# Performance work log

Hardware: AMD Instinct MI355X
Metric: run time of the kernel (lower is better)

## Reference

```python
import jax, jax.numpy as jnp
import numpy as np

ALPHA = 2.0  # spikingjelly default ATan surrogate alpha
EPS = 1e-5   # BatchNorm eps

@jax.custom_vjp
def heaviside_atan(x):
    return (x >= 0.0).astype(x.dtype)

def _ha_fwd(x):
    return heaviside_atan(x), x

def _ha_bwd(x, g):
    return (g * ALPHA / (2.0 * (1.0 + (jnp.pi / 2.0 * ALPHA * x) ** 2)),)

heaviside_atan.defvjp(_ha_fwd, _ha_bwd)

def lif(x_seq, tau=2.0, v_th=1.0):
    # MultiStepLIFNode, v_reset=0 (hard reset), detach_reset=True
    def step(v, x):
        v = v + (x - v) / tau
        s = heaviside_atan(v - v_th)
        v = v * (1.0 - jax.lax.stop_gradient(s))
        return v, s
    _, spikes = jax.lax.scan(step, jnp.zeros_like(x_seq[0]), x_seq)
    return spikes

def conv_bn(y, Wt, g, b):
    # 1x1 conv (no bias) + BatchNorm2d in training mode over flattened (T*B, H, W)
    y = jnp.einsum('tbchw,oc->tbohw', y, Wt)
    m = y.mean(axis=(0, 1, 3, 4), keepdims=True)
    v = y.var(axis=(0, 1, 3, 4), keepdims=True)
    C = Wt.shape[0]
    return (y - m) / jnp.sqrt(v + EPS) * g.reshape(1, 1, C, 1, 1) + b.reshape(1, 1, C, 1, 1)

def setup_inputs() -> dict:
    key = jax.random.key(0)
    ks = jax.random.split(key, 5)
    T, B, C, H, W = 4, 64, 384, 14, 14
    x = jax.random.normal(ks[0], (T, B, C, H, W), dtype=jnp.float32)
    Wq = jax.random.normal(ks[1], (C, C), dtype=jnp.float32) * 0.02
    Wk = jax.random.normal(ks[2], (C, C), dtype=jnp.float32) * 0.02
    Wv = jax.random.normal(ks[3], (C, C), dtype=jnp.float32) * 0.02
    Wp = jax.random.normal(ks[4], (C, C), dtype=jnp.float32) * 0.02
    ones = jnp.ones((C,), jnp.float32)
    zeros = jnp.zeros((C,), jnp.float32)
    return {"x": x, "Wq": Wq, "Wk": Wk, "Wv": Wv, "Wp": Wp,
            "gq": ones, "bq": zeros, "gk": ones, "bk": zeros,
            "gv": ones, "bv": zeros, "gp": ones, "bp": zeros}

def reference(x, Wq, Wk, Wv, Wp, gq, bq, gk, bk, gv, bv, gp, bp):
    T, B, C, H, W = x.shape
    nh = 8
    dh = C // nh
    N = H * W

    xs = lif(x)  # pre_lif

    def heads(y):  # [T,B,C,H,W] -> [T,B,h,N,dh]
        y = y.reshape(T, B, C, N).transpose(0, 1, 3, 2)
        return y.reshape(T, B, N, nh, dh).transpose(0, 1, 3, 2, 4)

    q = heads(lif(conv_bn(xs, Wq, gq, bq)))
    k = heads(lif(conv_bn(xs, Wk, gk, bk)))
    v = heads(lif(conv_bn(xs, Wv, gv, bv)))

    attn = jnp.einsum('tbhnd,tbhmd->tbhnm', q, k)      # no softmax
    o = jnp.einsum('tbhnm,tbhmd->tbhnd', attn, v) * 0.125
    o = o.transpose(0, 1, 2, 4, 3).reshape(T, B, C, N).reshape(T, B, C, H, W)
    o = lif(o, v_th=0.5)                                # attn_lif
    return conv_bn(o, Wp, gp, bp)                       # proj (no lif)
```

## Files before the change

### kernel.cpp

```cpp
#include <hip/hip_runtime.h>
#include <hip/hip_bf16.h>
#include <stdint.h>

#define T_  4
#define B_  64
#define C_  384
#define N_  196
#define NH  8
#define DH  48
#define TB_ (T_*B_)
#define R_  (T_*B_*N_)
#define NW  12
#define P_  12544
#define SBLK1 3136
#define SA_  64

typedef float f32x2 __attribute__((ext_vector_type(2)));

__global__ void transpose_w4(const float* __restrict__ s0, const float* __restrict__ s1,
                             const float* __restrict__ s2, const float* __restrict__ s3,
                             float* __restrict__ dst){
    int m = blockIdx.y;
    const float* src = (m==0)?s0:(m==1)?s1:(m==2)?s2:s3;
    int idx = blockIdx.x*256 + threadIdx.x;
    if (idx >= C_*C_) return;
    int o = idx % C_, c = idx / C_;
    dst[(size_t)m*C_*C_ + idx] = src[o*C_ + c];
}

__global__ __launch_bounds__(256) void pre_lif(const float* __restrict__ x,
                                               uint32_t* __restrict__ maskXS){
    int b = blockIdx.x / NW;
    int w = blockIdx.x % NW;
    int n = threadIdx.x;
    if (n >= N_) return;
    float v[32];
#pragma unroll
    for (int j=0;j<32;j++) v[j] = 0.f;
#pragma unroll
    for (int t=0;t<T_;t++){
        uint32_t word = 0;
#pragma unroll
        for (int j=0;j<32;j++){
            int c = w*32 + j;
            float xv = x[((size_t)(t*B_+b)*C_ + c)*N_ + n];
            v[j] = v[j] + (xv - v[j])*0.5f;
            if (v[j] >= 1.0f){ word |= (1u<<j); v[j] = 0.f; }
        }
        maskXS[((size_t)(t*B_+b)*N_ + n)*NW + w] = word;
    }
}

__global__ __launch_bounds__(256) void conv_statsO(const uint32_t* __restrict__ mask,
                                                   const float* __restrict__ WT,
                                                   float* __restrict__ p1,
                                                   float* __restrict__ p2){
    __shared__ float red1[4][C_];
    __shared__ float red2[4][C_];
    int tid = threadIdx.x, wave = tid>>6, lane = tid&63;
    int ob = 6*lane;
    f32x2 s10={0.f,0.f}, s11={0.f,0.f}, s12={0.f,0.f};
    f32x2 s20={0.f,0.f}, s21={0.f,0.f}, s22={0.f,0.f};
    for (int p=0;p<4;p++){
        int pix = (blockIdx.x*4 + wave)*4 + p;
        const uint4* m4 = (const uint4*)(mask + (size_t)pix*NW);
        uint4 ma = m4[0], mb = m4[1], mc = m4[2];
        uint32_t mwv[12] = {ma.x,ma.y,ma.z,ma.w, mb.x,mb.y,mb.z,mb.w, mc.x,mc.y,mc.z,mc.w};
        f32x2 y0={0.f,0.f}, y1={0.f,0.f}, y2={0.f,0.f};
        f32x2 z0={0.f,0.f}, z1={0.f,0.f}, z2={0.f,0.f};
#pragma unroll
        for (int w=0; w<NW; w++){
            uint32_t bits = mwv[w];
            while (bits){
                int c0 = (w<<5) + __builtin_ctz(bits); bits &= bits-1;
                const f32x2* col0 = (const f32x2*)(WT + (size_t)c0*C_ + ob);
                if (bits){
                    int c1 = (w<<5) + __builtin_ctz(bits); bits &= bits-1;
                    const f32x2* col1 = (const f32x2*)(WT + (size_t)c1*C_ + ob);
                    f32x2 a0=col0[0],a1=col0[1],a2=col0[2];
                    f32x2 b0=col1[0],b1=col1[1],b2=col1[2];
                    y0+=a0; y1+=a1; y2+=a2;
                    z0+=b0; z1+=b1; z2+=b2;
                } else {
                    y0+=col0[0]; y1+=col0[1]; y2+=col0[2];
                }
            }
        }
        y0+=z0; y1+=z1; y2+=z2;
        s10+=y0; s11+=y1; s12+=y2;
        s20+=y0*y0; s21+=y1*y1; s22+=y2*y2;
    }
    *(f32x2*)&red1[wave][ob  ] = s10;
    *(f32x2*)&red1[wave][ob+2] = s11;
    *(f32x2*)&red1[wave][ob+4] = s12;
    *(f32x2*)&red2[wave][ob  ] = s20;
    *(f32x2*)&red2[wave][ob+2] = s21;
    *(f32x2*)&red2[wave][ob+4] = s22;
    __syncthreads();
    for (int i=tid; i<C_; i+=256){
        p1[(size_t)blockIdx.x*C_ + i] = (red1[0][i]+red1[1][i])+(red1[2][i]+red1[3][i]);
        p2[(size_t)blockIdx.x*C_ + i] = (red2[0][i]+red2[1][i])+(red2[2][i]+red2[3][i]);
    }
}

__global__ __launch_bounds__(384) void statsA(const float* __restrict__ p1,
                                              const float* __restrict__ p2,
                                              float* __restrict__ q1,
                                              float* __restrict__ q2){
    int o = threadIdx.x;
    int blk = blockIdx.x;
    const int ROWS = SBLK1 / SA_;
    size_t base = (size_t)blk*ROWS*C_ + o;
    float s1=0.f, s2=0.f;
#pragma unroll 4
    for (int r=0;r<ROWS;r++){
        s1 += p1[base + (size_t)r*C_];
        s2 += p2[base + (size_t)r*C_];
    }
    q1[blk*C_ + o] = s1;
    q2[blk*C_ + o] = s2;
}

__global__ __launch_bounds__(384) void statsB(const float* __restrict__ q1,
                                              const float* __restrict__ q2,
                                              const float* __restrict__ g,
                                              const float* __restrict__ bta,
                                              float* __restrict__ scale,
                                              float* __restrict__ shift){
    int o = threadIdx.x;
    float s1=0.f, s2=0.f;
#pragma unroll
    for (int b=0;b<SA_;b++){ s1 += q1[b*C_+o]; s2 += q2[b*C_+o]; }
    float m   = s1 / (float)R_;
    float var = s2 / (float)R_ - m*m;
    float sc  = g[o] / sqrtf(var + 1e-5f);
    scale[o] = sc;
    shift[o] = bta[o] - m*sc;
}

__global__ __launch_bounds__(256) void conv_lif(const uint32_t* __restrict__ mask,
                                                const float* __restrict__ WT,
                                                const float* __restrict__ scale,
                                                const float* __restrict__ shift,
                                                uint32_t* __restrict__ mo){
    int tid = threadIdx.x, wave = tid>>6, lane = tid&63;
    int pix0 = blockIdx.x*4 + wave;
    float sc[6], sh[6], v[6];
#pragma unroll
    for (int i=0;i<6;i++){
        sc[i] = scale[(i<<6)+lane];
        sh[i] = shift[(i<<6)+lane];
        v[i]  = 0.f;
    }
    for (int t=0;t<T_;t++){
        size_t pix = (size_t)t*P_ + pix0;
        const uint4* m4 = (const uint4*)(mask + pix*NW);
        uint4 ma = m4[0], mb = m4[1], mc = m4[2];
        uint32_t mwv[12] = {ma.x,ma.y,ma.z,ma.w, mb.x,mb.y,mb.z,mb.w, mc.x,mc.y,mc.z,mc.w};
        float y[6] = {0.f,0.f,0.f,0.f,0.f,0.f};
        float z[6] = {0.f,0.f,0.f,0.f,0.f,0.f};
#pragma unroll
        for (int w=0; w<NW; w++){
            uint32_t bits = mwv[w];
            while (bits){
                int c0 = (w<<5) + __builtin_ctz(bits); bits &= bits-1;
                const float* col0 = WT + (size_t)c0*C_ + lane;
                if (bits){
                    int c1 = (w<<5) + __builtin_ctz(bits); bits &= bits-1;
                    const float* col1 = WT + (size_t)c1*C_ + lane;
#pragma unroll
                    for (int i=0;i<6;i++){ y[i]+=col0[i<<6]; z[i]+=col1[i<<6]; }
                } else {
#pragma unroll
                    for (int i=0;i<6;i++) y[i]+=col0[i<<6];
                }
            }
        }
        uint32_t words[12];
#pragma unroll
        for (int i=0;i<6;i++){
            float val = (y[i]+z[i])*sc[i] + sh[i];
            v[i] = v[i] + (val - v[i])*0.5f;
            int s = (v[i] >= 1.0f);
            unsigned long long bal = __ballot(s);
            if (s) v[i] = 0.f;
            words[2*i]   = (uint32_t)bal;
            words[2*i+1] = (uint32_t)(bal>>32);
        }
        if (lane == 0){
            uint4* o4 = (uint4*)(mo + pix*NW);
            o4[0] = make_uint4(words[0],words[1],words[2],words[3]);
            o4[1] = make_uint4(words[4],words[5],words[6],words[7]);
            o4[2] = make_uint4(words[8],words[9],words[10],words[11]);
        }
    }
}

__global__ __launch_bounds__(256) void attention_lif(const uint32_t* __restrict__ mq,
                                                     const uint32_t* __restrict__ mk,
                                                     const uint32_t* __restrict__ mv,
                                                     uint16_t* __restrict__ mo){
    __shared__ unsigned long long kT[DH][4];
    __shared__ unsigned long long vT[DH][4];
    __shared__ uint32_t Cp[DH*25];

    int h = blockIdx.x & 7;
    int b = blockIdx.x >> 3;
    int tid = threadIdx.x, wv = tid>>6, lane = tid&63;
    int sw  = (h*DH) >> 5;
    int shf = (h*DH) & 31;

    float vm[DH];
#pragma unroll
    for (int d=0;d<DH;d++) vm[d] = 0.f;

    for (int t=0;t<T_;t++){
        int tb = t*B_ + b;
        unsigned long long q = 0, kk = 0, vvv = 0;
        if (tid < N_){
            const uint32_t* pq = mq + ((size_t)tb*N_ + tid)*NW + sw;
            const uint32_t* pk = mk + ((size_t)tb*N_ + tid)*NW + sw;
            const uint32_t* pv = mv + ((size_t)tb*N_ + tid)*NW + sw;
            unsigned long long lo, hi;
            lo = pq[0]; hi = pq[1];
            q   = (shf ? ((lo>>16) | (hi<<16)) : (lo | (hi<<32))) & 0xFFFFFFFFFFFFULL;
            lo = pk[0]; hi = pk[1];
            kk  = (shf ? ((lo>>16) | (hi<<16)) : (lo | (hi<<32))) & 0xFFFFFFFFFFFFULL;
            lo = pv[0]; hi = pv[1];
            vvv = (shf ? ((lo>>16) | (hi<<16)) : (lo | (hi<<32))) & 0xFFFFFFFFFFFFULL;
        }
#pragma unroll 1
        for (int d=0; d<DH; d++){
            unsigned long long bk_ = __ballot((int)((kk >>d)&1ull));
            unsigned long long bv_ = __ballot((int)((vvv>>d)&1ull));
            if (lane == 0){ kT[d][wv] = bk_; vT[d][wv] = bv_; }
        }
        __syncthreads();

        if (tid < 240){
            int j  = tid / 5;
            int dg = tid % 5;
            int d0 = dg*10;
            int d1 = (dg==4) ? 48 : d0+10;
            unsigned long long ka=kT[j][0], kb=kT[j][1], kc=kT[j][2], kd=kT[j][3];
            for (int d=d0; d<d1; d+=2){
                uint32_t c0 = (uint32_t)(__popcll(ka&vT[d][0]) + __popcll(kb&vT[d][1])
                            + __popcll(kc&vT[d][2]) + __popcll(kd&vT[d][3]));
                uint32_t c1 = (uint32_t)(__popcll(ka&vT[d+1][0]) + __popcll(kb&vT[d+1][1])
                            + __popcll(kc&vT[d+1][2]) + __popcll(kd&vT[d+1][3]));
                Cp[j*25 + (d>>1)] = c0 | (c1<<16);
            }
        }
        __syncthreads();

        if (tid < N_){
            uint32_t acc[24];
#pragma unroll
            for (int p=0;p<24;p++) acc[p] = 0u;
            unsigned long long qb = q;
            while (qb){
                int j = __builtin_ctzll(qb); qb &= qb-1;
                const uint32_t* row = &Cp[j*25];
#pragma unroll
                for (int p=0;p<24;p++) acc[p] += row[p];
            }
            unsigned long long sp = 0;
#pragma unroll
            for (int d=0; d<DH; d++){
                uint32_t a = (d&1) ? (acc[d>>1]>>16) : (acc[d>>1]&0xFFFFu);
                float o = 0.125f*(float)a;
                vm[d] = vm[d] + (o - vm[d])*0.5f;
                if (vm[d] >= 0.5f){ sp |= (1ull<<d); vm[d] = 0.f; }
            }
            size_t rec = ((size_t)tb*N_ + tid)*24 + 3*h;
            mo[rec]   = (uint16_t)(sp);
            mo[rec+1] = (uint16_t)(sp >> 16);
            mo[rec+2] = (uint16_t)(sp >> 32);
        }
        __syncthreads();
    }
}

__global__ __launch_bounds__(256) void proj_out(const uint32_t* __restrict__ mask,
                                                const float* __restrict__ WT,
                                                const float* __restrict__ scale,
                                                const float* __restrict__ shift,
                                                float* __restrict__ out){
    __shared__ float tile[192][98];
    int bid = blockIdx.x;
    int tb = bid>>2, nh = (bid>>1)&1, ch = bid&1;
    int n0 = nh*98, c0 = ch*192;
    int tid = threadIdx.x, wave = tid>>6, lane = tid&63;
    float sc[3], sh[3];
#pragma unroll
    for (int i=0;i<3;i++){
        sc[i] = scale[c0+(i<<6)+lane];
        sh[i] = shift[c0+(i<<6)+lane];
    }
    for (int p=wave; p<98; p+=4){
        size_t pix = (size_t)tb*N_ + n0 + p;
        const uint4* m4 = (const uint4*)(mask + pix*NW);
        uint4 ma = m4[0], mb = m4[1], mc = m4[2];
        uint32_t mwv[12] = {ma.x,ma.y,ma.z,ma.w, mb.x,mb.y,mb.z,mb.w, mc.x,mc.y,mc.z,mc.w};
        float y[3] = {0.f,0.f,0.f};
        float z[3] = {0.f,0.f,0.f};
#pragma unroll
        for (int w=0; w<NW; w++){
            uint32_t bits = mwv[w];
            while (bits){
                int cc0 = (w<<5) + __builtin_ctz(bits); bits &= bits-1;
                const float* col0 = WT + (size_t)cc0*C_ + c0 + lane;
                if (bits){
                    int cc1 = (w<<5) + __builtin_ctz(bits); bits &= bits-1;
                    const float* col1 = WT + (size_t)cc1*C_ + c0 + lane;
#pragma unroll
                    for (int i=0;i<3;i++){ y[i]+=col0[i<<6]; z[i]+=col1[i<<6]; }
                } else {
#pragma unroll
                    for (int i=0;i<3;i++) y[i]+=col0[i<<6];
                }
            }
        }
#pragma unroll
        for (int i=0;i<3;i++)
            tile[(i<<6)+lane][p] = (y[i]+z[i])*sc[i] + sh[i];
    }
    __syncthreads();
    for (int r=wave; r<192; r+=4){
        if (lane < 49){
            f32x2 tv = *(const f32x2*)&tile[r][2*lane];
            *(f32x2*)(out + ((size_t)tb*C_ + c0 + r)*N_ + n0 + 2*lane) = tv;
        }
    }
}

extern "C" void kernel_launch(void* const* d_in, const int* in_sizes, int n_in,
                              void* d_out, int out_size, void* d_ws, size_t ws_size,
                              hipStream_t stream) {
    const float* x  = (const float*)d_in[0];
    const float* Wq = (const float*)d_in[1];
    const float* Wk = (const float*)d_in[2];
    const float* Wv = (const float*)d_in[3];
    const float* Wp = (const float*)d_in[4];
    const float* gq = (const float*)d_in[5];
    const float* bq = (const float*)d_in[6];
    const float* gk = (const float*)d_in[7];
    const float* bk = (const float*)d_in[8];
    const float* gv = (const float*)d_in[9];
    const float* bv = (const float*)d_in[10];
    const float* gp = (const float*)d_in[11];
    const float* bp = (const float*)d_in[12];

    char* w = (char*)d_ws;
    size_t off = 0;
    uint32_t* maskXS = (uint32_t*)(w + off); off += (size_t)R_*NW*4;
    uint32_t* maskQ  = (uint32_t*)(w + off); off += (size_t)R_*NW*4;
    uint32_t* maskK  = (uint32_t*)(w + off); off += (size_t)R_*NW*4;
    uint32_t* maskV  = (uint32_t*)(w + off); off += (size_t)R_*NW*4;
    float* WTall = (float*)(w + off); off += (size_t)4*C_*C_*4;
    float* p1 = (float*)(w + off); off += (size_t)SBLK1*C_*4;
    float* p2 = (float*)(w + off); off += (size_t)SBLK1*C_*4;
    float* q1 = (float*)(w + off); off += (size_t)SA_*C_*4;
    float* q2 = (float*)(w + off); off += (size_t)SA_*C_*4;
    float* scaleB = (float*)(w + off); off += C_*4;
    float* shiftB = (float*)(w + off); off += C_*4;
    uint32_t* maskOL = maskXS;

    transpose_w4<<<dim3((C_*C_+255)/256, 4),256,0,stream>>>(Wq, Wk, Wv, Wp, WTall);

    pre_lif<<<B_*NW,256,0,stream>>>(x, maskXS);

    const float* Gs[3] = {gq, gk, gv};
    const float* Bs[3] = {bq, bk, bv};
    uint32_t* Ms[3] = {maskQ, maskK, maskV};
    for (int i=0;i<3;i++){
        const float* WT = WTall + (size_t)i*C_*C_;
        conv_statsO<<<SBLK1,256,0,stream>>>(maskXS, WT, p1, p2);
        statsA<<<SA_,384,0,stream>>>(p1, p2, q1, q2);
        statsB<<<1,384,0,stream>>>(q1, q2, Gs[i], Bs[i], scaleB, shiftB);
        conv_lif<<<P_/4,256,0,stream>>>(maskXS, WT, scaleB, shiftB, Ms[i]);
    }

    attention_lif<<<B_*NH,256,0,stream>>>(maskQ, maskK, maskV, (uint16_t*)maskOL);

    const float* WTp = WTall + (size_t)3*C_*C_;
    conv_statsO<<<SBLK1,256,0,stream>>>(maskOL, WTp, p1, p2);
    statsA<<<SA_,384,0,stream>>>(p1, p2, q1, q2);
    statsB<<<1,384,0,stream>>>(q1, q2, gp, bp, scaleB, shiftB);

    proj_out<<<TB_*4,256,0,stream>>>(maskOL, WTp, scaleB, shiftB, (float*)d_out);
}
```

Measured before the change: 445.8 us.

## Compute BatchNorm stats from binary spike Gram matrix instead of conv passes

Replaces the per-branch conv+stats passes with a bit-transposed spike mask and a popcount Gram matrix S^T S, shared by the Q/K/V branches. Mean and variance of each conv output channel then come from W·G·W^T and the spike counts, so the input is read once rather than three times. conv_lif is batched across the three branches in one launch, and both conv kernels now build a shared-memory list of active channel indices with 4-way accumulation. This adds new kernels, LDS atomics and a larger workspace. Computing variance as E[y^2]-m^2 in fp32 from Gram sums changes the rounding.

Result: faster. 422.6 us (-5.2%).

```diff
diff --git a/kernel.cpp b/kernel.cpp
--- a/kernel.cpp
+++ b/kernel.cpp
@@ -12,8 +12,8 @@
 #define R_  (T_*B_*N_)
 #define NW  12
 #define P_  12544
-#define SBLK1 3136
-#define SA_  64
+#define NCH 66
+#define KG_ 17
 
 typedef float f32x2 __attribute__((ext_vector_type(2)));
 
@@ -51,105 +51,149 @@
     }
 }
 
-__global__ __launch_bounds__(256) void conv_statsO(const uint32_t* __restrict__ mask,
-                                                   const float* __restrict__ WT,
-                                                   float* __restrict__ p1,
-                                                   float* __restrict__ p2){
-    __shared__ float red1[4][C_];
-    __shared__ float red2[4][C_];
+__global__ __launch_bounds__(256) void bit_transpose(const uint32_t* __restrict__ mask,
+                                                     unsigned long long* __restrict__ maskT){
+    int gw = blockIdx.x*4 + (threadIdx.x>>6);
+    int lane = threadIdx.x & 63;
+    int kc = gw/12, kw = gw%12;
+    uint32_t mwv[12];
+#pragma unroll
+    for (int w=0;w<12;w++) mwv[w]=0u;
+    if (gw < 784){
+        int pix = gw*64 + lane;
+        const uint4* m4 = (const uint4*)(mask + (size_t)pix*NW);
+        uint4 a=m4[0], b=m4[1], c=m4[2];
+        mwv[0]=a.x; mwv[1]=a.y; mwv[2]=a.z; mwv[3]=a.w;
+        mwv[4]=b.x; mwv[5]=b.y; mwv[6]=b.z; mwv[7]=b.w;
+        mwv[8]=c.x; mwv[9]=c.y; mwv[10]=c.z; mwv[11]=c.w;
+    }
+#pragma unroll
+    for (int w=0; w<12; w++){
+        uint32_t word = mwv[w];
+#pragma unroll
+        for (int j=0; j<32; j++){
+            unsigned long long bal = __ballot((int)((word>>j)&1u));
+            if (lane == 0)
+                maskT[((size_t)kc*C_ + (w*32+j))*12 + kw] = bal;
+        }
+    }
+}
+
+__global__ __launch_bounds__(256) void gram(const unsigned long long* __restrict__ maskT,
+                                            unsigned int* __restrict__ Gpart){
+    __shared__ unsigned int tile[64][49];
     int tid = threadIdx.x, wave = tid>>6, lane = tid&63;
-    int ob = 6*lane;
-    f32x2 s10={0.f,0.f}, s11={0.f,0.f}, s12={0.f,0.f};
-    f32x2 s20={0.f,0.f}, s21={0.f,0.f}, s22={0.f,0.f};
-    for (int p=0;p<4;p++){
-        int pix = (blockIdx.x*4 + wave)*4 + p;
-        const uint4* m4 = (const uint4*)(mask + (size_t)pix*NW);
-        uint4 ma = m4[0], mb = m4[1], mc = m4[2];
-        uint32_t mwv[12] = {ma.x,ma.y,ma.z,ma.w, mb.x,mb.y,mb.z,mb.w, mc.x,mc.y,mc.z,mc.w};
-        f32x2 y0={0.f,0.f}, y1={0.f,0.f}, y2={0.f,0.f};
-        f32x2 z0={0.f,0.f}, z1={0.f,0.f}, z2={0.f,0.f};
-#pragma unroll
-        for (int w=0; w<NW; w++){
-            uint32_t bits = mwv[w];
-            while (bits){
-                int c0 = (w<<5) + __builtin_ctz(bits); bits &= bits-1;
-                const f32x2* col0 = (const f32x2*)(WT + (size_t)c0*C_ + ob);
-                if (bits){
-                    int c1 = (w<<5) + __builtin_ctz(bits); bits &= bits-1;
-                    const f32x2* col1 = (const f32x2*)(WT + (size_t)c1*C_ + ob);
-                    f32x2 a0=col0[0],a1=col0[1],a2=col0[2];
-                    f32x2 b0=col1[0],b1=col1[1],b2=col1[2];
-                    y0+=a0; y1+=a1; y2+=a2;
-                    z0+=b0; z1+=b1; z2+=b2;
-                } else {
-                    y0+=col0[0]; y1+=col0[1]; y2+=col0[2];
-                }
-            }
-        }
-        y0+=z0; y1+=z1; y2+=z2;
-        s10+=y0; s11+=y1; s12+=y2;
-        s20+=y0*y0; s21+=y1*y1; s22+=y2*y2;
-    }
-    *(f32x2*)&red1[wave][ob  ] = s10;
-    *(f32x2*)&red1[wave][ob+2] = s11;
-    *(f32x2*)&red1[wave][ob+4] = s12;
-    *(f32x2*)&red2[wave][ob  ] = s20;
-    *(f32x2*)&red2[wave][ob+2] = s21;
-    *(f32x2*)&red2[wave][ob+4] = s22;
+    int kg = blockIdx.x, rg = blockIdx.y, cg = blockIdx.z;
+    for (int i=tid; i<64*49; i+=256) ((unsigned int*)tile)[i] = 0u;
     __syncthreads();
-    for (int i=tid; i<C_; i+=256){
-        p1[(size_t)blockIdx.x*C_ + i] = (red1[0][i]+red1[1][i])+(red1[2][i]+red1[3][i]);
-        p2[(size_t)blockIdx.x*C_ + i] = (red2[0][i]+red2[1][i])+(red2[2][i]+red2[3][i]);
-    }
-}
-
-__global__ __launch_bounds__(384) void statsA(const float* __restrict__ p1,
-                                              const float* __restrict__ p2,
-                                              float* __restrict__ q1,
-                                              float* __restrict__ q2){
-    int o = threadIdx.x;
-    int blk = blockIdx.x;
-    const int ROWS = SBLK1 / SA_;
-    size_t base = (size_t)blk*ROWS*C_ + o;
-    float s1=0.f, s2=0.f;
+    int kc = kg*4 + wave;
+    if (kc < NCH){
+        const uint4* rp = (const uint4*)(maskT + ((size_t)kc*C_ + rg*64 + lane)*12);
+        uint32_t row[24];
+#pragma unroll
+        for (int q=0;q<6;q++){
+            uint4 a = rp[q];
+            row[4*q]=a.x; row[4*q+1]=a.y; row[4*q+2]=a.z; row[4*q+3]=a.w;
+        }
+        for (int cc=0; cc<48; cc++){
+            const uint4* cp = (const uint4*)(maskT + ((size_t)kc*C_ + cg*48 + cc)*12);
+            uint32_t col[24];
+#pragma unroll
+            for (int q=0;q<6;q++){
+                uint4 a = cp[q];
+                col[4*q]=a.x; col[4*q+1]=a.y; col[4*q+2]=a.z; col[4*q+3]=a.w;
+            }
+            unsigned int s = 0;
+#pragma unroll
+            for (int q=0;q<24;q++) s += (unsigned int)__popc(row[q]&col[q]);
+            atomicAdd(&tile[lane][cc], s);
+        }
+    }
+    __syncthreads();
+    unsigned int* out = Gpart + (size_t)kg*C_*C_;
+    for (int i=tid; i<64*48; i+=256){
+        int r = i/48, cc = i%48;
+        out[(size_t)(rg*64+r)*C_ + cg*48 + cc] = tile[r][cc];
+    }
+}
+
+__global__ __launch_bounds__(256) void gram_reduce(const unsigned int* __restrict__ Gpart,
+                                                   float* __restrict__ Gf){
+    int e = blockIdx.x*256 + threadIdx.x;
+    unsigned int s = 0;
+#pragma unroll
+    for (int k=0;k<KG_;k++) s += Gpart[(size_t)k*C_*C_ + e];
+    Gf[e] = (float)s;
+}
+
+__global__ __launch_bounds__(384) void bn_from_gram(const float* __restrict__ Gf,
+        const float* __restrict__ WTall,
+        const float* __restrict__ g0, const float* __restrict__ b0,
+        const float* __restrict__ g1, const float* __restrict__ b1,
+        const float* __restrict__ g2, const float* __restrict__ b2,
+        float* __restrict__ scaleOut, float* __restrict__ shiftOut, int wtBase){
+    __shared__ float w4[384][4];
+    __shared__ float sred[8][6];
+    int t = threadIdx.x, wave = t>>6, lane = t&63;
+    int br = blockIdx.y;
+    const float* WT = WTall + (size_t)(wtBase+br)*C_*C_;
+    int o0 = blockIdx.x*4;
+    float4 wv = *(const float4*)(WT + (size_t)t*C_ + o0);
+    w4[t][0]=wv.x; w4[t][1]=wv.y; w4[t][2]=wv.z; w4[t][3]=wv.w;
+    __syncthreads();
+    float h0=0.f,h1=0.f,h2=0.f,h3=0.f;
 #pragma unroll 4
-    for (int r=0;r<ROWS;r++){
-        s1 += p1[base + (size_t)r*C_];
-        s2 += p2[base + (size_t)r*C_];
-    }
-    q1[blk*C_ + o] = s1;
-    q2[blk*C_ + o] = s2;
-}
-
-__global__ __launch_bounds__(384) void statsB(const float* __restrict__ q1,
-                                              const float* __restrict__ q2,
-                                              const float* __restrict__ g,
-                                              const float* __restrict__ bta,
-                                              float* __restrict__ scale,
-                                              float* __restrict__ shift){
-    int o = threadIdx.x;
-    float s1=0.f, s2=0.f;
-#pragma unroll
-    for (int b=0;b<SA_;b++){ s1 += q1[b*C_+o]; s2 += q2[b*C_+o]; }
-    float m   = s1 / (float)R_;
-    float var = s2 / (float)R_ - m*m;
-    float sc  = g[o] / sqrtf(var + 1e-5f);
-    scale[o] = sc;
-    shift[o] = bta[o] - m*sc;
+    for (int c=0;c<C_;c++){
+        float gv = Gf[(size_t)c*C_ + t];
+        float4 wc = *(const float4*)&w4[c][0];
+        h0 += gv*wc.x; h1 += gv*wc.y; h2 += gv*wc.z; h3 += gv*wc.w;
+    }
+    float cnt = Gf[(size_t)t*C_ + t];
+    float p0=wv.x*h0, p1=wv.y*h1, p2=wv.z*h2, p3=wv.w*h3;
+    float q0=cnt*wv.x, q1=cnt*wv.y, q2=cnt*wv.z, q3=cnt*wv.w;
+#pragma unroll
+    for (int off=32; off>0; off>>=1){
+        p0+=__shfl_down(p0,off); p1+=__shfl_down(p1,off);
+        p2+=__shfl_down(p2,off); p3+=__shfl_down(p3,off);
+        q0+=__shfl_down(q0,off); q1+=__shfl_down(q1,off);
+        q2+=__shfl_down(q2,off); q3+=__shfl_down(q3,off);
+    }
+    if (lane == 0){
+        sred[0][wave]=p0; sred[1][wave]=p1; sred[2][wave]=p2; sred[3][wave]=p3;
+        sred[4][wave]=q0; sred[5][wave]=q1; sred[6][wave]=q2; sred[7][wave]=q3;
+    }
+    __syncthreads();
+    if (t < 4){
+        const float* g  = (br==0)?g0:(br==1)?g1:g2;
+        const float* bb = (br==0)?b0:(br==1)?b1:b2;
+        float ss = ((sred[t][0]+sred[t][1])+(sred[t][2]+sred[t][3]))+(sred[t][4]+sred[t][5]);
+        float sm = ((sred[4+t][0]+sred[4+t][1])+(sred[4+t][2]+sred[4+t][3]))+(sred[4+t][4]+sred[4+t][5]);
+        float m   = sm / (float)R_;
+        float var = ss / (float)R_ - m*m;
+        float sc  = g[o0+t] / sqrtf(var + 1e-5f);
+        scaleOut[br*C_ + o0+t] = sc;
+        shiftOut[br*C_ + o0+t] = bb[o0+t] - m*sc;
+    }
 }
 
 __global__ __launch_bounds__(256) void conv_lif(const uint32_t* __restrict__ mask,
-                                                const float* __restrict__ WT,
-                                                const float* __restrict__ scale,
-                                                const float* __restrict__ shift,
-                                                uint32_t* __restrict__ mo){
+                                                const float* __restrict__ WTall,
+                                                const float* __restrict__ scaleAll,
+                                                const float* __restrict__ shiftAll,
+                                                uint32_t* __restrict__ moQ,
+                                                uint32_t* __restrict__ moK,
+                                                uint32_t* __restrict__ moV){
+    __shared__ uint16_t lst[4][400];
+    int br = blockIdx.y;
+    const float* WT = WTall + (size_t)br*C_*C_;
+    uint32_t* mo = (br==0)?moQ:(br==1)?moK:moV;
     int tid = threadIdx.x, wave = tid>>6, lane = tid&63;
     int pix0 = blockIdx.x*4 + wave;
     float sc[6], sh[6], v[6];
 #pragma unroll
     for (int i=0;i<6;i++){
-        sc[i] = scale[(i<<6)+lane];
-        sh[i] = shift[(i<<6)+lane];
+        sc[i] = scaleAll[br*C_ + (i<<6) + lane];
+        sh[i] = shiftAll[br*C_ + (i<<6) + lane];
         v[i]  = 0.f;
     }
     for (int t=0;t<T_;t++){
@@ -157,35 +201,51 @@
         const uint4* m4 = (const uint4*)(mask + pix*NW);
         uint4 ma = m4[0], mb = m4[1], mc = m4[2];
         uint32_t mwv[12] = {ma.x,ma.y,ma.z,ma.w, mb.x,mb.y,mb.z,mb.w, mc.x,mc.y,mc.z,mc.w};
-        float y[6] = {0.f,0.f,0.f,0.f,0.f,0.f};
-        float z[6] = {0.f,0.f,0.f,0.f,0.f,0.f};
-#pragma unroll
-        for (int w=0; w<NW; w++){
-            uint32_t bits = mwv[w];
-            while (bits){
-                int c0 = (w<<5) + __builtin_ctz(bits); bits &= bits-1;
-                const float* col0 = WT + (size_t)c0*C_ + lane;
-                if (bits){
-                    int c1 = (w<<5) + __builtin_ctz(bits); bits &= bits-1;
-                    const float* col1 = WT + (size_t)c1*C_ + lane;
-#pragma unroll
-                    for (int i=0;i<6;i++){ y[i]+=col0[i<<6]; z[i]+=col1[i<<6]; }
-                } else {
-#pragma unroll
-                    for (int i=0;i<6;i++) y[i]+=col0[i<<6];
+        int cnt = 0;
+#pragma unroll
+        for (int w=0;w<12;w++) cnt += __popc(mwv[w]);
+        if (lane == 0){
+            int k = 0;
+#pragma unroll
+            for (int w=0;w<12;w++){
+                uint32_t bits = mwv[w];
+                while (bits){
+                    lst[wave][k++] = (uint16_t)((w<<5) + __builtin_ctz(bits));
+                    bits &= bits - 1;
                 }
             }
         }
+        float ya[6]={0,0,0,0,0,0}, yb[6]={0,0,0,0,0,0};
+        float yc[6]={0,0,0,0,0,0}, yd[6]={0,0,0,0,0,0};
+        int i = 0;
+        for (; i+3 < cnt; i += 4){
+            ushort4 cs = *(const ushort4*)&lst[wave][i];
+            const float* q0 = WT + (size_t)cs.x*C_ + lane;
+            const float* q1 = WT + (size_t)cs.y*C_ + lane;
+            const float* q2 = WT + (size_t)cs.z*C_ + lane;
+            const float* q3 = WT + (size_t)cs.w*C_ + lane;
+#pragma unroll
+            for (int j=0;j<6;j++){
+                ya[j] += q0[j<<6]; yb[j] += q1[j<<6];
+                yc[j] += q2[j<<6]; yd[j] += q3[j<<6];
+            }
+        }
+        for (; i < cnt; ++i){
+            int c = lst[wave][i];
+            const float* q0 = WT + (size_t)c*C_ + lane;
+#pragma unroll
+            for (int j=0;j<6;j++) ya[j] += q0[j<<6];
+        }
         uint32_t words[12];
 #pragma unroll
-        for (int i=0;i<6;i++){
-            float val = (y[i]+z[i])*sc[i] + sh[i];
-            v[i] = v[i] + (val - v[i])*0.5f;
-            int s = (v[i] >= 1.0f);
+        for (int j=0;j<6;j++){
+            float val = ((ya[j]+yb[j]) + (yc[j]+yd[j]))*sc[j] + sh[j];
+            v[j] = v[j] + (val - v[j])*0.5f;
+            int s = (v[j] >= 1.0f);
             unsigned long long bal = __ballot(s);
-            if (s) v[i] = 0.f;
-            words[2*i]   = (uint32_t)bal;
-            words[2*i+1] = (uint32_t)(bal>>32);
+            if (s) v[j] = 0.f;
+            words[2*j]   = (uint32_t)bal;
+            words[2*j+1] = (uint32_t)(bal>>32);
         }
         if (lane == 0){
             uint4* o4 = (uint4*)(mo + pix*NW);
@@ -287,6 +347,7 @@
                                                 const float* __restrict__ shift,
                                                 float* __restrict__ out){
     __shared__ float tile[192][98];
+    __shared__ uint16_t lst[4][400];
     int bid = blockIdx.x;
     int tb = bid>>2, nh = (bid>>1)&1, ch = bid&1;
     int n0 = nh*98, c0 = ch*192;
@@ -302,28 +363,43 @@
         const uint4* m4 = (const uint4*)(mask + pix*NW);
         uint4 ma = m4[0], mb = m4[1], mc = m4[2];
         uint32_t mwv[12] = {ma.x,ma.y,ma.z,ma.w, mb.x,mb.y,mb.z,mb.w, mc.x,mc.y,mc.z,mc.w};
-        float y[3] = {0.f,0.f,0.f};
-        float z[3] = {0.f,0.f,0.f};
-#pragma unroll
-        for (int w=0; w<NW; w++){
-            uint32_t bits = mwv[w];
-            while (bits){
-                int cc0 = (w<<5) + __builtin_ctz(bits); bits &= bits-1;
-                const float* col0 = WT + (size_t)cc0*C_ + c0 + lane;
-                if (bits){
-                    int cc1 = (w<<5) + __builtin_ctz(bits); bits &= bits-1;
-                    const float* col1 = WT + (size_t)cc1*C_ + c0 + lane;
-#pragma unroll
-                    for (int i=0;i<3;i++){ y[i]+=col0[i<<6]; z[i]+=col1[i<<6]; }
-                } else {
-#pragma unroll
-                    for (int i=0;i<3;i++) y[i]+=col0[i<<6];
+        int cnt = 0;
+#pragma unroll
+        for (int w=0;w<12;w++) cnt += __popc(mwv[w]);
+        if (lane == 0){
+            int k = 0;
+#pragma unroll
+            for (int w=0;w<12;w++){
+                uint32_t bits = mwv[w];
+                while (bits){
+                    lst[wave][k++] = (uint16_t)((w<<5) + __builtin_ctz(bits));
+                    bits &= bits - 1;
                 }
             }
         }
-#pragma unroll
-        for (int i=0;i<3;i++)
-            tile[(i<<6)+lane][p] = (y[i]+z[i])*sc[i] + sh[i];
+        float ya[3]={0,0,0}, yb[3]={0,0,0}, yc[3]={0,0,0}, yd[3]={0,0,0};
+        int i = 0;
+        for (; i+3 < cnt; i += 4){
+            ushort4 cs = *(const ushort4*)&lst[wave][i];
+            const float* q0 = WT + (size_t)cs.x*C_ + c0 + lane;
+            const float* q1 = WT + (size_t)cs.y*C_ + c0 + lane;
+            const float* q2 = WT + (size_t)cs.z*C_ + c0 + lane;
+            const float* q3 = WT + (size_t)cs.w*C_ + c0 + lane;
+#pragma unroll
+            for (int j=0;j<3;j++){
+                ya[j] += q0[j<<6]; yb[j] += q1[j<<6];
+                yc[j] += q2[j<<6]; yd[j] += q3[j<<6];
+            }
+        }
+        for (; i < cnt; ++i){
+            int c = lst[wave][i];
+            const float* q0 = WT + (size_t)c*C_ + c0 + lane;
+#pragma unroll
+            for (int j=0;j<3;j++) ya[j] += q0[j<<6];
+        }
+#pragma unroll
+        for (int j=0;j<3;j++)
+            tile[(j<<6)+lane][p] = ((ya[j]+yb[j])+(yc[j]+yd[j]))*sc[j] + sh[j];
     }
     __syncthreads();
     for (int r=wave; r<192; r+=4){
@@ -358,35 +434,34 @@
     uint32_t* maskK  = (uint32_t*)(w + off); off += (size_t)R_*NW*4;
     uint32_t* maskV  = (uint32_t*)(w + off); off += (size_t)R_*NW*4;
     float* WTall = (float*)(w + off); off += (size_t)4*C_*C_*4;
-    float* p1 = (float*)(w + off); off += (size_t)SBLK1*C_*4;
-    float* p2 = (float*)(w + off); off += (size_t)SBLK1*C_*4;
-    float* q1 = (float*)(w + off); off += (size_t)SA_*C_*4;
-    float* q2 = (float*)(w + off); off += (size_t)SA_*C_*4;
-    float* scaleB = (float*)(w + off); off += C_*4;
-    float* shiftB = (float*)(w + off); off += C_*4;
+    unsigned long long* maskT = (unsigned long long*)(w + off); off += (size_t)NCH*C_*12*8;
+    unsigned int* Gpart = (unsigned int*)(w + off); off += (size_t)KG_*C_*C_*4;
+    float* Gf = (float*)(w + off); off += (size_t)C_*C_*4;
+    float* scaleB = (float*)(w + off); off += (size_t)4*C_*4;
+    float* shiftB = (float*)(w + off); off += (size_t)4*C_*4;
     uint32_t* maskOL = maskXS;
 
     transpose_w4<<<dim3((C_*C_+255)/256, 4),256,0,stream>>>(Wq, Wk, Wv, Wp, WTall);
 
     pre_lif<<<B_*NW,256,0,stream>>>(x, maskXS);
 
-    const float* Gs[3] = {gq, gk, gv};
-    const float* Bs[3] = {bq, bk, bv};
-    uint32_t* Ms[3] = {maskQ, maskK, maskV};
-    for (int i=0;i<3;i++){
-        const float* WT = WTall + (size_t)i*C_*C_;
-        conv_statsO<<<SBLK1,256,0,stream>>>(maskXS, WT, p1, p2);
-        statsA<<<SA_,384,0,stream>>>(p1, p2, q1, q2);
-        statsB<<<1,384,0,stream>>>(q1, q2, Gs[i], Bs[i], scaleB, shiftB);
-        conv_lif<<<P_/4,256,0,stream>>>(maskXS, WT, scaleB, shiftB, Ms[i]);
-    }
+    bit_transpose<<<198,256,0,stream>>>(maskXS, maskT);
+    gram<<<dim3(KG_,6,8),256,0,stream>>>(maskT, Gpart);
+    gram_reduce<<<576,256,0,stream>>>(Gpart, Gf);
+    bn_from_gram<<<dim3(96,3),384,0,stream>>>(Gf, WTall, gq,bq, gk,bk, gv,bv,
+                                              scaleB, shiftB, 0);
+
+    conv_lif<<<dim3(P_/4,3),256,0,stream>>>(maskXS, WTall, scaleB, shiftB,
+                                            maskQ, maskK, maskV);
 
     attention_lif<<<B_*NH,256,0,stream>>>(maskQ, maskK, maskV, (uint16_t*)maskOL);
 
-    const float* WTp = WTall + (size_t)3*C_*C_;
-    conv_statsO<<<SBLK1,256,0,stream>>>(maskOL, WTp, p1, p2);
-    statsA<<<SA_,384,0,stream>>>(p1, p2, q1, q2);
-    statsB<<<1,384,0,stream>>>(q1, q2, gp, bp, scaleB, shiftB);
-
-    proj_out<<<TB_*4,256,0,stream>>>(maskOL, WTp, scaleB, shiftB, (float*)d_out);
-}
+    bit_transpose<<<198,256,0,stream>>>(maskOL, maskT);
+    gram<<<dim3(KG_,6,8),256,0,stream>>>(maskT, Gpart);
+    gram_reduce<<<576,256,0,stream>>>(Gpart, Gf);
+    bn_from_gram<<<dim3(96,1),384,0,stream>>>(Gf, WTall, gp,bp, gp,bp, gp,bp,
+                                              scaleB + 3*C_, shiftB + 3*C_, 3);
+
+    proj_out<<<TB_*4,256,0,stream>>>(maskOL, WTall + (size_t)3*C_*C_,
+                                     scaleB + 3*C_, shiftB + 3*C_, (float*)d_out);
+}
```
